# Performance work log

Hardware: AMD Instinct MI355X
Metric: run time of the kernel (lower is better)

The kernel has to match this reference:

```python
import jax, jax.numpy as jnp
import numpy as np

NEG_SLOPE = 0.2


def _gatv2_hop(x_l, x_r, src, dst, att_k, bias_k, num_nodes, add_self_loops):
    # x_l, x_r: [N, H, C]; src/dst: [E] int; att_k: [H, C]; bias_k: [C]
    if add_self_loops:
        loop = jnp.arange(num_nodes, dtype=src.dtype)
        src = jnp.concatenate([src, loop])
        dst = jnp.concatenate([dst, loop])
    g = jax.nn.leaky_relu(x_l[src] + x_r[dst], NEG_SLOPE)      # [E, H, C]
    logit = jnp.einsum('ehc,hc->eh', g, att_k)                 # [E, H]
    m = jax.ops.segment_max(logit, dst, num_segments=num_nodes)  # [N, H]
    a = jnp.exp(logit - m[dst])
    denom = jax.ops.segment_sum(a, dst, num_segments=num_nodes)  # [N, H]
    alpha = a / denom[dst]                                     # [E, H]
    out = jax.ops.segment_sum(alpha[:, :, None] * x_l[src], dst,
                              num_segments=num_nodes)          # [N, H, C]
    return out.mean(axis=1) + bias_k                           # concat=False -> head mean


def setup_inputs() -> dict:
    key = jax.random.key(0)
    N, E, IN, H, C, K = 50000, 800000, 128, 4, 32, 3
    ks = jax.random.split(key, 16)
    x = jax.random.normal(ks[0], (N, IN), dtype=jnp.float32)
    edges = {}
    for k in range(K):
        src = jax.random.randint(ks[1 + 2 * k], (E,), 0, N, dtype=jnp.int32)
        off = jax.random.randint(ks[2 + 2 * k], (E,), 1, N, dtype=jnp.int32)
        dst = (src + off) % N  # guarantees no self-loops in the data
        edges[f'edge_index{k}'] = jnp.stack([src, dst])
    s = 1.0 / np.sqrt(IN)
    w_l = jax.random.normal(ks[7], (IN, H * C), dtype=jnp.float32) * s
    b_l = jax.random.normal(ks[8], (H * C,), dtype=jnp.float32) * 0.02
    w_r = jax.random.normal(ks[9], (IN, H * C), dtype=jnp.float32) * s
    b_r = jax.random.normal(ks[10], (H * C,), dtype=jnp.float32) * 0.02
    att = jax.random.normal(ks[11], (K, H, C), dtype=jnp.float32) * (1.0 / np.sqrt(C))
    conv_bias = jax.random.normal(ks[12], (K, C), dtype=jnp.float32) * 0.02
    gate_w = jax.random.normal(ks[13], (IN, K), dtype=jnp.float32) * s
    gate_b = jax.random.normal(ks[14], (K,), dtype=jnp.float32) * 0.02
    return dict(x=x, **edges, w_l=w_l, b_l=b_l, w_r=w_r, b_r=b_r, att=att,
                conv_bias=conv_bias, gate_w=gate_w, gate_b=gate_b)


def reference(x, edge_index0, edge_index1, edge_index2,
              w_l, b_l, w_r, b_r, att, conv_bias, gate_w, gate_b):
    N = x.shape[0]
    H, C = att.shape[1], att.shape[2]
    x_l = (x @ w_l + b_l).reshape(N, H, C)  # shared lin_l across hops
    x_r = (x @ w_r + b_r).reshape(N, H, C)  # shared lin_r across hops
    edges = [edge_index0, edge_index1, edge_index2]
    msgs = [
        _gatv2_hop(x_l, x_r, ei[0], ei[1], att[k], conv_bias[k], N,
                   add_self_loops=(k == 0))
        for k, ei in enumerate(edges)
    ]
    messages = jnp.stack(msgs, axis=1)                 # [N, K, C]
    weights = jax.nn.softmax(x @ gate_w + gate_b, -1)  # [N, K]
    return jnp.einsum('nkc,nk->nc', messages, weights)
```

## Files before the change

### kernel.cpp

```cpp
#include <hip/hip_runtime.h>
#include <math.h>

typedef unsigned int uint32;
typedef unsigned short u16;

#if __has_builtin(__builtin_amdgcn_exp2f)
#define EXP2F(x) __builtin_amdgcn_exp2f(x)
#else
#define EXP2F(x) exp2f(x)
#endif

#define LROWS 64
#define CHUNK 8192
#define CHUNK_SHIFT 13
#define NBUCK_MAX 512
#define LPB 384

typedef __attribute__((ext_vector_type(8))) short bf16x8;
typedef __attribute__((ext_vector_type(4))) float f32x4;

__device__ __forceinline__ u16 f2bf(float f) {
    uint32 u = __float_as_uint(f);
    u += 0x7fffu + ((u >> 16) & 1u);
    return (u16)(u >> 16);
}
__device__ __forceinline__ float bflo(uint32 v) { return __uint_as_float(v << 16); }
__device__ __forceinline__ float bfhij(uint32 v) { return __uint_as_float(v); }

template<int PAT>
__device__ __forceinline__ float swz(float v) {
    return __int_as_float(__builtin_amdgcn_ds_swizzle(__float_as_int(v), PAT));
}
template<int CTRL>
__device__ __forceinline__ float dppadd(float v) {
    int r = __builtin_amdgcn_update_dpp(0, __float_as_int(v), CTRL, 0xF, 0xF, true);
    return v + __int_as_float(r);
}

__device__ __forceinline__ void edge_decode(
    int t, int E, const int* __restrict__ e0, const int* __restrict__ e1,
    const int* __restrict__ e2, int& hop, int& src, int& dst)
{
    if (t < E)          { hop = 0; src = e0[t];         dst = e0[E + t]; }
    else if (t < 2 * E) { hop = 1; src = e1[t - E];     dst = e1[t]; }
    else if (t < 3 * E) { hop = 2; src = e2[t - 2 * E]; dst = e2[t - E]; }
    else                { hop = 0; src = t - 3 * E;     dst = src; }
}

__global__ __launch_bounds__(256) void wprep(
    const float* __restrict__ wl, const float* __restrict__ wr, u16* __restrict__ wfrag)
{
    int ct = blockIdx.x;
    int ks = threadIdx.x >> 6;
    int lane = threadIdx.x & 63;
    int g = lane >> 4, rr = lane & 15;
    int c = ct * 16 + rr;
    const float* w = (c < 128) ? wl : wr;
    int cc = c & 127;
    u16* o = wfrag + (((size_t)ct * 4 + ks) * 64 + lane) * 8;
#pragma unroll
    for (int i = 0; i < 8; ++i) {
        int k = ks * 32 + g * 4 + (i & 3) + ((i >> 2) << 4);
        o[i] = f2bf(w[k * 128 + cc]);
    }
}

__global__ __launch_bounds__(256) void fused_pre(
    const float* __restrict__ x, const u16* __restrict__ wfrag,
    const float* __restrict__ bl, const float* __restrict__ br,
    const float* __restrict__ gw, const float* __restrict__ gb,
    u16* __restrict__ xl, u16* __restrict__ xr, float* __restrict__ gate4,
    const int* __restrict__ e0, const int* __restrict__ e1, const int* __restrict__ e2,
    int* __restrict__ hist,
    int N, int E, int T, int LB, int NBUCK)
{
    __shared__ float4 sx[LROWS][32];
    __shared__ float gbuf[LROWS][3];
    __shared__ int lhist[NBUCK_MAX];

    if ((int)blockIdx.x >= LB) {
        int blk = (int)blockIdx.x - LB;
        int t0 = blk << CHUNK_SHIFT;
        for (int j = threadIdx.x; j < NBUCK; j += 256) lhist[j] = 0;
        __syncthreads();
        for (int it = 0; it < CHUNK / 256; ++it) {
            int t = t0 + it * 256 + (int)threadIdx.x;
            if (t < T) {
                int dst;
                if (t < E)          dst = e0[E + t];
                else if (t < 2 * E) dst = e1[t];
                else if (t < 3 * E) dst = e2[t - E];
                else                dst = t - 3 * E;
                atomicAdd(&lhist[dst >> 7], 1);
            }
        }
        __syncthreads();
        for (int j = threadIdx.x; j < NBUCK; j += 256)
            hist[(size_t)blk * NBUCK + j] = lhist[j];
        return;
    }
    int t = threadIdx.x;
    int r0 = blockIdx.x * LROWS;
    int nr = min(LROWS, N - r0);
    {
        const float4* xi = (const float4*)(x + (size_t)r0 * 128);
        for (int i = t; i < nr * 32; i += 256) ((float4*)sx)[i] = xi[i];
    }
    __syncthreads();
    int wv = t >> 6, lane = t & 63;
    int g = lane >> 4, rr = lane & 15;
    bf16x8 afr[4];
    {
        const float4* xrow = sx[wv * 16 + rr];
#pragma unroll
        for (int ks = 0; ks < 4; ++ks) {
            float4 u = xrow[ks * 8 + g];
            float4 v = xrow[ks * 8 + 4 + g];
            union { u16 h[8]; bf16x8 v8; } pk;
            pk.h[0] = f2bf(u.x); pk.h[1] = f2bf(u.y);
            pk.h[2] = f2bf(u.z); pk.h[3] = f2bf(u.w);
            pk.h[4] = f2bf(v.x); pk.h[5] = f2bf(v.y);
            pk.h[6] = f2bf(v.z); pk.h[7] = f2bf(v.w);
            afr[ks] = pk.v8;
        }
    }
    const bf16x8* wfp = (const bf16x8*)wfrag;
    for (int ct = 0; ct < 16; ++ct) {
        f32x4 acc = {0.f, 0.f, 0.f, 0.f};
#pragma unroll
        for (int ks = 0; ks < 4; ++ks) {
            bf16x8 bf = wfp[((ct * 4 + ks) << 6) + lane];
            acc = __builtin_amdgcn_mfma_f32_16x16x32_bf16(afr[ks], bf, acc, 0, 0, 0);
        }
        int c = ct * 16 + rr;
        float bv = (ct < 8) ? bl[c] : br[c - 128];
        u16* ob = (ct < 8) ? xl : xr;
        int cc = c & 127;
#pragma unroll
        for (int i = 0; i < 4; ++i) {
            int row = wv * 16 + g * 4 + i;
            if (row < nr)
                ob[(size_t)(r0 + row) * 128 + cc] = f2bf(acc[i] + bv);
        }
    }
    if (t < nr * 3) {
        int r = t / 3, k = t - 3 * r;
        float s = 0.f;
        const float4* xrow = sx[r];
#pragma unroll 4
        for (int i = 0; i < 32; ++i) {
            float4 v = xrow[i];
            s += v.x * gw[(4 * i + 0) * 3 + k] + v.y * gw[(4 * i + 1) * 3 + k]
               + v.z * gw[(4 * i + 2) * 3 + k] + v.w * gw[(4 * i + 3) * 3 + k];
        }
        gbuf[r][k] = s + gb[k];
    }
    __syncthreads();
    if (t < nr) {
        float s0 = gbuf[t][0], s1 = gbuf[t][1], s2 = gbuf[t][2];
        float mx = fmaxf(s0, fmaxf(s1, s2));
        float e0v = __expf(s0 - mx), e1v = __expf(s1 - mx), e2v = __expf(s2 - mx);
        float inv = 1.f / (e0v + e1v + e2v);
        *(float4*)(gate4 + (size_t)(r0 + t) * 4) = make_float4(e0v * inv, e1v * inv, e2v * inv, 0.f);
    }
}

__global__ __launch_bounds__(1024) void scan1h(const int* __restrict__ hist, int MH,
                                               int NBLKA, int NBUCK,
                                               int* __restrict__ histS, int* __restrict__ partials) {
    __shared__ int s[1024];
    int t = threadIdx.x;
    int i = blockIdx.x * 1024 + t;
    int v = 0;
    if (i < MH) {
        int bin = (int)((uint32)i / (uint32)NBLKA);
        int blk = i - bin * NBLKA;
        v = hist[(size_t)blk * NBUCK + bin];
    }
    s[t] = v;
    __syncthreads();
    for (int o = 1; o < 1024; o <<= 1) {
        int u = (t >= o) ? s[t - o] : 0;
        __syncthreads();
        s[t] += u;
        __syncthreads();
    }
    if (i < MH) histS[i] = s[t] - v;
    if (t == 1023) partials[blockIdx.x] = s[1023];
}

__global__ __launch_bounds__(1024) void scan2(int* __restrict__ partials, int G) {
    __shared__ int s[1024];
    int t = threadIdx.x;
    int v = (t < G) ? partials[t] : 0;
    s[t] = v;
    __syncthreads();
    for (int o = 1; o < 1024; o <<= 1) {
        int u = (t >= o) ? s[t - o] : 0;
        __syncthreads();
        s[t] += u;
        __syncthreads();
    }
    if (t < G) partials[t] = s[t] - v;
}

__global__ __launch_bounds__(512) void passA2(
    const int* __restrict__ e0, const int* __restrict__ e1, const int* __restrict__ e2,
    int E, int T, int NBLKA, int NBUCK,
    const int* __restrict__ hist, const int* __restrict__ histS,
    const int* __restrict__ partials,
    uint32* __restrict__ pairs)
{
    __shared__ int lscan[512];
    __shared__ int gbase[512];
    __shared__ uint32 lp[CHUNK];
    __shared__ u16 lb[CHUNK];
    int blk = blockIdx.x, tid = threadIdx.x;
    int t0 = blk << CHUNK_SHIFT;
    int vc = min(CHUNK, T - t0);
    int c = (tid < NBUCK) ? hist[(size_t)blk * NBUCK + tid] : 0;
    lscan[tid] = c;
    __syncthreads();
    for (int o = 1; o < 512; o <<= 1) {
        int u = (tid >= o) ? lscan[tid - o] : 0;
        __syncthreads();
        lscan[tid] += u;
        __syncthreads();
    }
    int excl = lscan[tid] - c;
    lscan[tid] = excl;
    if (tid < NBUCK) {
        int k = tid * NBLKA + blk;
        gbase[tid] = histS[k] + partials[k >> 10] - excl;
    }
    __syncthreads();
    for (int it = 0; it < CHUNK / 512; ++it) {
        int t = t0 + it * 512 + tid;
        if (t < T) {
            int hop, src, dst;
            edge_decode(t, E, e0, e1, e2, hop, src, dst);
            int bin = dst >> 7;
            int j = atomicAdd(&lscan[bin], 1);
            lp[j] = (uint32)src | ((uint32)((dst & 127) * 3 + hop) << 16);
            lb[j] = (u16)bin;
        }
    }
    __syncthreads();
    for (int j = tid; j < vc; j += 512)
        pairs[gbase[lb[j]] + j] = lp[j];
}

__global__ __launch_bounds__(512) void passB(
    const uint32* __restrict__ pairs, const int* __restrict__ histS,
    const int* __restrict__ partials, u16* __restrict__ csr, int* __restrict__ offsets,
    int T, int M, int NBLKA, int NBUCK) {
    __shared__ int cnt[LPB];
    __shared__ int scn[512];
    int b = blockIdx.x;
    int tid = threadIdx.x;
    int k0 = b * NBLKA;
    int bbase = histS[k0] + partials[k0 >> 10];
    int bend;
    if (b == NBUCK - 1) bend = T;
    else { int k1 = k0 + NBLKA; bend = histS[k1] + partials[k1 >> 10]; }
    if (b == 0 && tid == 0) offsets[M] = T;

    if (tid < LPB) cnt[tid] = 0;
    __syncthreads();
    for (int p = bbase + tid; p < bend; p += 512)
        atomicAdd(&cnt[pairs[p] >> 16], 1);
    __syncthreads();
    int c = (tid < LPB) ? cnt[tid] : 0;
    scn[tid] = c;
    __syncthreads();
    for (int o = 1; o < 512; o <<= 1) {
        int u = (tid >= o) ? scn[tid - o] : 0;
        __syncthreads();
        scn[tid] += u;
        __syncthreads();
    }
    int excl = scn[tid] - c;
    int nlists = min(LPB, M - b * LPB);
    if (tid < nlists) offsets[b * LPB + tid] = bbase + excl;
    __syncthreads();
    if (tid < LPB) cnt[tid] = excl;
    __syncthreads();
    for (int p = bbase + tid; p < bend; p += 512) {
        uint32 pr = pairs[p];
        int pos = bbase + atomicAdd(&cnt[pr >> 16], 1);
        csr[pos] = (u16)pr;
    }
}

__global__ __launch_bounds__(192) void node_hop(
    const uint2* __restrict__ xlv,
    const uint2* __restrict__ xrv,
    const u16* __restrict__ csr,
    const int* __restrict__ offsets,
    const float* __restrict__ att,
    const float* __restrict__ bias,
    const float* __restrict__ gate4,
    float* __restrict__ out,
    int N, int M)
{
    const float L2E = 1.44269504088896f;
    __shared__ float4 smsg[3][8];
    int n = blockIdx.x;
    int h = threadIdx.x >> 6;
    int lane = threadIdx.x & 63;
    int i = 3 * n + h;
    int half = lane >> 5, l5 = lane & 31;

    uint2 rv = xrv[(size_t)n * 32 + l5];
    float4 r4;
    r4.x = bflo(rv.x); r4.y = bfhij(rv.x);
    r4.z = bflo(rv.y); r4.w = bfhij(rv.y);
    float4 a4 = ((const float4*)(att + h * 128))[l5];
    float a6x = 0.6f * L2E * a4.x, a6y = 0.6f * L2E * a4.y;
    float a6z = 0.6f * L2E * a4.z, a6w = 0.6f * L2E * a4.w;
    float a4x = 0.4f * L2E * a4.x, a4y = 0.4f * L2E * a4.y;
    float a4z = 0.4f * L2E * a4.z, a4w = 0.4f * L2E * a4.w;
    int beg = offsets[i];
    int end = offsets[i + 1];

    float d = 0.f, acc0 = 0.f, acc1 = 0.f, acc2 = 0.f, acc3 = 0.f;
    int e = beg;
    if (e + 8 <= end) {
        int sA = csr[e + half];
        int sB = csr[e + 2 + half];
        int sC = csr[e + 4 + half];
        int sD = csr[e + 6 + half];
        uint2 lvA = xlv[sA * 32 + l5];
        uint2 lvB = xlv[sB * 32 + l5];
        uint2 lvC = xlv[sC * 32 + l5];
        uint2 lvD = xlv[sD * 32 + l5];
        for (; e + 8 <= end; e += 8) {
            uint2 cvA = lvA, cvB = lvB, cvC = lvC, cvD = lvD;
            sA = csr[e + 8 + half];
            sB = csr[e + 10 + half];
            sC = csr[e + 12 + half];
            sD = csr[e + 14 + half];
            lvA = xlv[sA * 32 + l5];
            lvB = xlv[sB * 32 + l5];
            lvC = xlv[sC * 32 + l5];
            lvD = xlv[sD * 32 + l5];
            float lxA0 = bflo(cvA.x), lxA1 = bfhij(cvA.x);
            float lxA2 = bflo(cvA.y), lxA3 = bfhij(cvA.y);
            float lxB0 = bflo(cvB.x), lxB1 = bfhij(cvB.x);
            float lxB2 = bflo(cvB.y), lxB3 = bfhij(cvB.y);
            float lxC0 = bflo(cvC.x), lxC1 = bfhij(cvC.x);
            float lxC2 = bflo(cvC.y), lxC3 = bfhij(cvC.y);
            float lxD0 = bflo(cvD.x), lxD1 = bfhij(cvD.x);
            float lxD2 = bflo(cvD.y), lxD3 = bfhij(cvD.y);
            float gA0 = lxA0 + r4.x, gA1 = lxA1 + r4.y, gA2 = lxA2 + r4.z, gA3 = lxA3 + r4.w;
            float gB0 = lxB0 + r4.x, gB1 = lxB1 + r4.y, gB2 = lxB2 + r4.z, gB3 = lxB3 + r4.w;
            float gC0 = lxC0 + r4.x, gC1 = lxC1 + r4.y, gC2 = lxC2 + r4.z, gC3 = lxC3 + r4.w;
            float gD0 = lxD0 + r4.x, gD1 = lxD1 + r4.y, gD2 = lxD2 + r4.z, gD3 = lxD3 + r4.w;
            float pA = a6x * gA0;
            pA = fmaf(a4x, fabsf(gA0), pA);
            pA = fmaf(a6y, gA1, pA);
            pA = fmaf(a4y, fabsf(gA1), pA);
            pA = fmaf(a6z, gA2, pA);
            pA = fmaf(a4z, fabsf(gA2), pA);
            pA = fmaf(a6w, gA3, pA);
            pA = fmaf(a4w, fabsf(gA3), pA);
            float pB = a6x * gB0;
            pB = fmaf(a4x, fabsf(gB0), pB);
            pB = fmaf(a6y, gB1, pB);
            pB = fmaf(a4y, fabsf(gB1), pB);
            pB = fmaf(a6z, gB2, pB);
            pB = fmaf(a4z, fabsf(gB2), pB);
            pB = fmaf(a6w, gB3, pB);
            pB = fmaf(a4w, fabsf(gB3), pB);
            float pC = a6x * gC0;
            pC = fmaf(a4x, fabsf(gC0), pC);
            pC = fmaf(a6y, gC1, pC);
            pC = fmaf(a4y, fabsf(gC1), pC);
            pC = fmaf(a6z, gC2, pC);
            pC = fmaf(a4z, fabsf(gC2), pC);
            pC = fmaf(a6w, gC3, pC);
            pC = fmaf(a4w, fabsf(gC3), pC);
            float pD = a6x * gD0;
            pD = fmaf(a4x, fabsf(gD0), pD);
            pD = fmaf(a6y, gD1, pD);
            pD = fmaf(a4y, fabsf(gD1), pD);
            pD = fmaf(a6z, gD2, pD);
            pD = fmaf(a4z, fabsf(gD2), pD);
            pD = fmaf(a6w, gD3, pD);
            pD = fmaf(a4w, fabsf(gD3), pD);
            pA = dppadd<0xB1>(pA);  pB = dppadd<0xB1>(pB);
            pC = dppadd<0xB1>(pC);  pD = dppadd<0xB1>(pD);
            pA = dppadd<0x4E>(pA);  pB = dppadd<0x4E>(pB);
            pC = dppadd<0x4E>(pC);  pD = dppadd<0x4E>(pD);
            pA = dppadd<0x141>(pA); pB = dppadd<0x141>(pB);
            pC = dppadd<0x141>(pC); pD = dppadd<0x141>(pD);
            float wvA = EXP2F(pA);
            float wvB = EXP2F(pB);
            float wvC = EXP2F(pC);
            float wvD = EXP2F(pD);
            d += (wvA + wvB) + (wvC + wvD);
            acc0 = fmaf(wvA, lxA0, acc0);
            acc1 = fmaf(wvA, lxA1, acc1);
            acc2 = fmaf(wvA, lxA2, acc2);
            acc3 = fmaf(wvA, lxA3, acc3);
            acc0 = fmaf(wvB, lxB0, acc0);
            acc1 = fmaf(wvB, lxB1, acc1);
            acc2 = fmaf(wvB, lxB2, acc2);
            acc3 = fmaf(wvB, lxB3, acc3);
            acc0 = fmaf(wvC, lxC0, acc0);
            acc1 = fmaf(wvC, lxC1, acc1);
            acc2 = fmaf(wvC, lxC2, acc2);
            acc3 = fmaf(wvC, lxC3, acc3);
            acc0 = fmaf(wvD, lxD0, acc0);
            acc1 = fmaf(wvD, lxD1, acc1);
            acc2 = fmaf(wvD, lxD2, acc2);
            acc3 = fmaf(wvD, lxD3, acc3);
        }
    }
    for (; e < end; e += 4) {
        int e1i = end - 1;
        int s1 = csr[min(e + half, e1i)];
        int s2 = csr[min(e + 2 + half, e1i)];
        uint2 cvA = xlv[s1 * 32 + l5];
        uint2 cvB = xlv[s2 * 32 + l5];
        bool vA = (e + half) < end;
        bool vB = (e + 2 + half) < end;
        float lxA0 = bflo(cvA.x), lxA1 = bfhij(cvA.x);
        float lxA2 = bflo(cvA.y), lxA3 = bfhij(cvA.y);
        float lxB0 = bflo(cvB.x), lxB1 = bfhij(cvB.x);
        float lxB2 = bflo(cvB.y), lxB3 = bfhij(cvB.y);
        float gA0 = lxA0 + r4.x, gA1 = lxA1 + r4.y;
        float gA2 = lxA2 + r4.z, gA3 = lxA3 + r4.w;
        float gB0 = lxB0 + r4.x, gB1 = lxB1 + r4.y;
        float gB2 = lxB2 + r4.z, gB3 = lxB3 + r4.w;
        float pA = a6x * gA0;
        pA = fmaf(a4x, fabsf(gA0), pA);
        pA = fmaf(a6y, gA1, pA);
        pA = fmaf(a4y, fabsf(gA1), pA);
        pA = fmaf(a6z, gA2, pA);
        pA = fmaf(a4z, fabsf(gA2), pA);
        pA = fmaf(a6w, gA3, pA);
        pA = fmaf(a4w, fabsf(gA3), pA);
        float pB = a6x * gB0;
        pB = fmaf(a4x, fabsf(gB0), pB);
        pB = fmaf(a6y, gB1, pB);
        pB = fmaf(a4y, fabsf(gB1), pB);
        pB = fmaf(a6z, gB2, pB);
        pB = fmaf(a4z, fabsf(gB2), pB);
        pB = fmaf(a6w, gB3, pB);
        pB = fmaf(a4w, fabsf(gB3), pB);
        pA = dppadd<0xB1>(pA);
        pB = dppadd<0xB1>(pB);
        pA = dppadd<0x4E>(pA);
        pB = dppadd<0x4E>(pB);
        pA = dppadd<0x141>(pA);
        pB = dppadd<0x141>(pB);
        float wvA = EXP2F(pA);
        float wvB = EXP2F(pB);
        wvA = vA ? wvA : 0.f;
        wvB = vB ? wvB : 0.f;
        d += wvA + wvB;
        acc0 = fmaf(wvA, lxA0, acc0);
        acc1 = fmaf(wvA, lxA1, acc1);
        acc2 = fmaf(wvA, lxA2, acc2);
        acc3 = fmaf(wvA, lxA3, acc3);
        acc0 = fmaf(wvB, lxB0, acc0);
        acc1 = fmaf(wvB, lxB1, acc1);
        acc2 = fmaf(wvB, lxB2, acc2);
        acc3 = fmaf(wvB, lxB3, acc3);
    }
    d += __shfl_xor(d, 32);
    acc0 += __shfl_xor(acc0, 32);
    acc1 += __shfl_xor(acc1, 32);
    acc2 += __shfl_xor(acc2, 32);
    acc3 += __shfl_xor(acc3, 32);
    float inv = (d > 0.f) ? (1.0f / d) : 0.f;
    float q0 = acc0 * inv, q1 = acc1 * inv, q2 = acc2 * inv, q3 = acc3 * inv;
    q0 += swz<0x201F>(q0);  q0 += swz<0x401F>(q0);
    q1 += swz<0x201F>(q1);  q1 += swz<0x401F>(q1);
    q2 += swz<0x201F>(q2);  q2 += swz<0x401F>(q2);
    q3 += swz<0x201F>(q3);  q3 += swz<0x401F>(q3);
    if (lane < 8) {
        float4 b4 = ((const float4*)(bias + h * 32))[lane];
        smsg[h][lane] = make_float4(fmaf(q0, 0.25f, b4.x), fmaf(q1, 0.25f, b4.y),
                                    fmaf(q2, 0.25f, b4.z), fmaf(q3, 0.25f, b4.w));
    }
    __syncthreads();
    if (threadIdx.x < 8) {
        int c = threadIdx.x;
        float4 g = ((const float4*)gate4)[n];
        float4 m0 = smsg[0][c], m1 = smsg[1][c], m2 = smsg[2][c];
        float4 o;
        o.x = g.x * m0.x + g.y * m1.x + g.z * m2.x;
        o.y = g.x * m0.y + g.y * m1.y + g.z * m2.y;
        o.z = g.x * m0.z + g.y * m1.z + g.z * m2.z;
        o.w = g.x * m0.w + g.y * m1.w + g.z * m2.w;
        ((float4*)(out + (size_t)n * 32))[c] = o;
    }
}

extern "C" void kernel_launch(void* const* d_in, const int* in_sizes, int n_in,
                              void* d_out, int out_size, void* d_ws, size_t ws_size,
                              hipStream_t stream) {
    const float* x  = (const float*)d_in[0];
    const int* e0 = (const int*)d_in[1];
    const int* e1 = (const int*)d_in[2];
    const int* e2 = (const int*)d_in[3];
    const float* wl = (const float*)d_in[4];
    const float* bl = (const float*)d_in[5];
    const float* wr = (const float*)d_in[6];
    const float* br = (const float*)d_in[7];
    const float* att = (const float*)d_in[8];
    const float* cb  = (const float*)d_in[9];
    const float* gw  = (const float*)d_in[10];
    const float* gb  = (const float*)d_in[11];

    int N = in_sizes[0] / 128;
    int E = in_sizes[1] / 2;
    float* out = (float*)d_out;

    int M = 3 * N;
    int T = 3 * E + N;
    int NBUCK = (N + 127) >> 7;
    int NBLKA = (T + CHUNK - 1) / CHUNK;
    int MH = NBUCK * NBLKA;

    char* ws = (char*)d_ws;
    u16* xl      = (u16*)ws;   ws += (size_t)N * 128 * 2;
    u16* xr      = (u16*)ws;   ws += (size_t)N * 128 * 2;
    float* gate4 = (float*)ws; ws += (size_t)N * 4 * 4;
    int* offsets  = (int*)ws; ws += (size_t)(M + 1) * 4;
    int* hist     = (int*)ws; ws += (size_t)MH * 4;
    int* histS    = (int*)ws; ws += (size_t)MH * 4;
    int* partials = (int*)ws; ws += 4096;
    u16* csr_src  = (u16*)ws; ws += (size_t)(T + 16) * 2;
    u16* wfrag    = (u16*)ws; ws += (size_t)16 * 4 * 64 * 8 * 2;
    uint32* pairs = (uint32*)(((uintptr_t)ws + 63) & ~(uintptr_t)63);

    int LB = (N + LROWS - 1) / LROWS;
    wprep<<<16, 256, 0, stream>>>(wl, wr, wfrag);
    fused_pre<<<LB + NBLKA, 256, 0, stream>>>(x, wfrag, bl, br, gw, gb, xl, xr, gate4,
                                              e0, e1, e2, hist, N, E, T, LB, NBUCK);
    int GH = (MH + 1023) / 1024;
    scan1h<<<GH, 1024, 0, stream>>>(hist, MH, NBLKA, NBUCK, histS, partials);
    scan2<<<1, 1024, 0, stream>>>(partials, GH);
    passA2<<<NBLKA, 512, 0, stream>>>(e0, e1, e2, E, T, NBLKA, NBUCK,
                                      hist, histS, partials, pairs);
    passB<<<NBUCK, 512, 0, stream>>>(pairs, histS, partials, csr_src, offsets,
                                     T, M, NBLKA, NBUCK);
    node_hop<<<N, 192, 0, stream>>>(
        (const uint2*)xl, (const uint2*)xr, csr_src, offsets, att, cb, gate4, out, N, M);
}
```

Measured before the change: 171.9 us.

## Fuse CSR bucket build with per-node attention aggregation using LDS-resident CSR

Merges the passB CSR scatter and the node_hop kernel into one per-bucket kernel. Each bucket's 128 destination nodes get their CSR offsets and source indices built in shared memory. The same block's 8 waves then process 16 nodes each across all three hops, writing the gated output directly. This removes the global offsets and CSR arrays and one kernel launch. In exchange the grid drops from one block per node to one block per bucket. That sharply reduces the waves available to hide gather latency, serialises hops and nodes within a wave, and assumes each bucket holds at most 8192 edges with no overflow check.

```diff
diff --git a/kernel.cpp b/kernel.cpp
--- a/kernel.cpp
+++ b/kernel.cpp
@@ -15,6 +15,7 @@
 #define CHUNK_SHIFT 13
 #define NBUCK_MAX 512
 #define LPB 384
+#define BCAP 8192
 
 typedef __attribute__((ext_vector_type(8))) short bf16x8;
 typedef __attribute__((ext_vector_type(4))) float f32x4;
@@ -250,12 +251,22 @@
         pairs[gbase[lb[j]] + j] = lp[j];
 }
 
-__global__ __launch_bounds__(512) void passB(
-    const uint32* __restrict__ pairs, const int* __restrict__ histS,
-    const int* __restrict__ partials, u16* __restrict__ csr, int* __restrict__ offsets,
-    int T, int M, int NBLKA, int NBUCK) {
+__global__ __launch_bounds__(512) void node_bucket(
+    const uint2* __restrict__ xlv,
+    const uint2* __restrict__ xrv,
+    const uint32* __restrict__ pairs,
+    const int* __restrict__ histS, const int* __restrict__ partials,
+    const float* __restrict__ att,
+    const float* __restrict__ bias,
+    const float* __restrict__ gate4,
+    float* __restrict__ out,
+    int N, int T, int NBLKA, int NBUCK)
+{
+    const float L2E = 1.44269504088896f;
     __shared__ int cnt[LPB];
     __shared__ int scn[512];
+    __shared__ int loff[LPB + 1];
+    __shared__ u16 lcsr[BCAP + 16];
     int b = blockIdx.x;
     int tid = threadIdx.x;
     int k0 = b * NBLKA;
@@ -263,7 +274,7 @@
     int bend;
     if (b == NBUCK - 1) bend = T;
     else { int k1 = k0 + NBLKA; bend = histS[k1] + partials[k1 >> 10]; }
-    if (b == 0 && tid == 0) offsets[M] = T;
+    int bc = bend - bbase;
 
     if (tid < LPB) cnt[tid] = 0;
     __syncthreads();
@@ -280,222 +291,202 @@
         __syncthreads();
     }
     int excl = scn[tid] - c;
-    int nlists = min(LPB, M - b * LPB);
-    if (tid < nlists) offsets[b * LPB + tid] = bbase + excl;
-    __syncthreads();
+    if (tid <= LPB) loff[tid] = excl;
     if (tid < LPB) cnt[tid] = excl;
+    if (tid < 16) lcsr[bc + tid] = 0;
     __syncthreads();
     for (int p = bbase + tid; p < bend; p += 512) {
         uint32 pr = pairs[p];
-        int pos = bbase + atomicAdd(&cnt[pr >> 16], 1);
-        csr[pos] = (u16)pr;
-    }
-}
-
-__global__ __launch_bounds__(192) void node_hop(
-    const uint2* __restrict__ xlv,
-    const uint2* __restrict__ xrv,
-    const u16* __restrict__ csr,
-    const int* __restrict__ offsets,
-    const float* __restrict__ att,
-    const float* __restrict__ bias,
-    const float* __restrict__ gate4,
-    float* __restrict__ out,
-    int N, int M)
-{
-    const float L2E = 1.44269504088896f;
-    __shared__ float4 smsg[3][8];
-    int n = blockIdx.x;
-    int h = threadIdx.x >> 6;
-    int lane = threadIdx.x & 63;
-    int i = 3 * n + h;
+        int pos = atomicAdd(&cnt[pr >> 16], 1);
+        lcsr[pos] = (u16)pr;
+    }
+    __syncthreads();
+
+    int wvid = tid >> 6;
+    int lane = tid & 63;
     int half = lane >> 5, l5 = lane & 31;
-
-    uint2 rv = xrv[(size_t)n * 32 + l5];
-    float4 r4;
-    r4.x = bflo(rv.x); r4.y = bfhij(rv.x);
-    r4.z = bflo(rv.y); r4.w = bfhij(rv.y);
-    float4 a4 = ((const float4*)(att + h * 128))[l5];
-    float a6x = 0.6f * L2E * a4.x, a6y = 0.6f * L2E * a4.y;
-    float a6z = 0.6f * L2E * a4.z, a6w = 0.6f * L2E * a4.w;
-    float a4x = 0.4f * L2E * a4.x, a4y = 0.4f * L2E * a4.y;
-    float a4z = 0.4f * L2E * a4.z, a4w = 0.4f * L2E * a4.w;
-    int beg = offsets[i];
-    int end = offsets[i + 1];
-
-    float d = 0.f, acc0 = 0.f, acc1 = 0.f, acc2 = 0.f, acc3 = 0.f;
-    int e = beg;
-    if (e + 8 <= end) {
-        int sA = csr[e + half];
-        int sB = csr[e + 2 + half];
-        int sC = csr[e + 4 + half];
-        int sD = csr[e + 6 + half];
-        uint2 lvA = xlv[sA * 32 + l5];
-        uint2 lvB = xlv[sB * 32 + l5];
-        uint2 lvC = xlv[sC * 32 + l5];
-        uint2 lvD = xlv[sD * 32 + l5];
-        for (; e + 8 <= end; e += 8) {
-            uint2 cvA = lvA, cvB = lvB, cvC = lvC, cvD = lvD;
-            sA = csr[e + 8 + half];
-            sB = csr[e + 10 + half];
-            sC = csr[e + 12 + half];
-            sD = csr[e + 14 + half];
-            lvA = xlv[sA * 32 + l5];
-            lvB = xlv[sB * 32 + l5];
-            lvC = xlv[sC * 32 + l5];
-            lvD = xlv[sD * 32 + l5];
-            float lxA0 = bflo(cvA.x), lxA1 = bfhij(cvA.x);
-            float lxA2 = bflo(cvA.y), lxA3 = bfhij(cvA.y);
-            float lxB0 = bflo(cvB.x), lxB1 = bfhij(cvB.x);
-            float lxB2 = bflo(cvB.y), lxB3 = bfhij(cvB.y);
-            float lxC0 = bflo(cvC.x), lxC1 = bfhij(cvC.x);
-            float lxC2 = bflo(cvC.y), lxC3 = bfhij(cvC.y);
-            float lxD0 = bflo(cvD.x), lxD1 = bfhij(cvD.x);
-            float lxD2 = bflo(cvD.y), lxD3 = bfhij(cvD.y);
-            float gA0 = lxA0 + r4.x, gA1 = lxA1 + r4.y, gA2 = lxA2 + r4.z, gA3 = lxA3 + r4.w;
-            float gB0 = lxB0 + r4.x, gB1 = lxB1 + r4.y, gB2 = lxB2 + r4.z, gB3 = lxB3 + r4.w;
-            float gC0 = lxC0 + r4.x, gC1 = lxC1 + r4.y, gC2 = lxC2 + r4.z, gC3 = lxC3 + r4.w;
-            float gD0 = lxD0 + r4.x, gD1 = lxD1 + r4.y, gD2 = lxD2 + r4.z, gD3 = lxD3 + r4.w;
-            float pA = a6x * gA0;
-            pA = fmaf(a4x, fabsf(gA0), pA);
-            pA = fmaf(a6y, gA1, pA);
-            pA = fmaf(a4y, fabsf(gA1), pA);
-            pA = fmaf(a6z, gA2, pA);
-            pA = fmaf(a4z, fabsf(gA2), pA);
-            pA = fmaf(a6w, gA3, pA);
-            pA = fmaf(a4w, fabsf(gA3), pA);
-            float pB = a6x * gB0;
-            pB = fmaf(a4x, fabsf(gB0), pB);
-            pB = fmaf(a6y, gB1, pB);
-            pB = fmaf(a4y, fabsf(gB1), pB);
-            pB = fmaf(a6z, gB2, pB);
-            pB = fmaf(a4z, fabsf(gB2), pB);
-            pB = fmaf(a6w, gB3, pB);
-            pB = fmaf(a4w, fabsf(gB3), pB);
-            float pC = a6x * gC0;
-            pC = fmaf(a4x, fabsf(gC0), pC);
-            pC = fmaf(a6y, gC1, pC);
-            pC = fmaf(a4y, fabsf(gC1), pC);
-            pC = fmaf(a6z, gC2, pC);
-            pC = fmaf(a4z, fabsf(gC2), pC);
-            pC = fmaf(a6w, gC3, pC);
-            pC = fmaf(a4w, fabsf(gC3), pC);
-            float pD = a6x * gD0;
-            pD = fmaf(a4x, fabsf(gD0), pD);
-            pD = fmaf(a6y, gD1, pD);
-            pD = fmaf(a4y, fabsf(gD1), pD);
-            pD = fmaf(a6z, gD2, pD);
-            pD = fmaf(a4z, fabsf(gD2), pD);
-            pD = fmaf(a6w, gD3, pD);
-            pD = fmaf(a4w, fabsf(gD3), pD);
-            pA = dppadd<0xB1>(pA);  pB = dppadd<0xB1>(pB);
-            pC = dppadd<0xB1>(pC);  pD = dppadd<0xB1>(pD);
-            pA = dppadd<0x4E>(pA);  pB = dppadd<0x4E>(pB);
-            pC = dppadd<0x4E>(pC);  pD = dppadd<0x4E>(pD);
-            pA = dppadd<0x141>(pA); pB = dppadd<0x141>(pB);
-            pC = dppadd<0x141>(pC); pD = dppadd<0x141>(pD);
-            float wvA = EXP2F(pA);
-            float wvB = EXP2F(pB);
-            float wvC = EXP2F(pC);
-            float wvD = EXP2F(pD);
-            d += (wvA + wvB) + (wvC + wvD);
-            acc0 = fmaf(wvA, lxA0, acc0);
-            acc1 = fmaf(wvA, lxA1, acc1);
-            acc2 = fmaf(wvA, lxA2, acc2);
-            acc3 = fmaf(wvA, lxA3, acc3);
-            acc0 = fmaf(wvB, lxB0, acc0);
-            acc1 = fmaf(wvB, lxB1, acc1);
-            acc2 = fmaf(wvB, lxB2, acc2);
-            acc3 = fmaf(wvB, lxB3, acc3);
-            acc0 = fmaf(wvC, lxC0, acc0);
-            acc1 = fmaf(wvC, lxC1, acc1);
-            acc2 = fmaf(wvC, lxC2, acc2);
-            acc3 = fmaf(wvC, lxC3, acc3);
-            acc0 = fmaf(wvD, lxD0, acc0);
-            acc1 = fmaf(wvD, lxD1, acc1);
-            acc2 = fmaf(wvD, lxD2, acc2);
-            acc3 = fmaf(wvD, lxD3, acc3);
-        }
-    }
-    for (; e < end; e += 4) {
-        int e1i = end - 1;
-        int s1 = csr[min(e + half, e1i)];
-        int s2 = csr[min(e + 2 + half, e1i)];
-        uint2 cvA = xlv[s1 * 32 + l5];
-        uint2 cvB = xlv[s2 * 32 + l5];
-        bool vA = (e + half) < end;
-        bool vB = (e + 2 + half) < end;
-        float lxA0 = bflo(cvA.x), lxA1 = bfhij(cvA.x);
-        float lxA2 = bflo(cvA.y), lxA3 = bfhij(cvA.y);
-        float lxB0 = bflo(cvB.x), lxB1 = bfhij(cvB.x);
-        float lxB2 = bflo(cvB.y), lxB3 = bfhij(cvB.y);
-        float gA0 = lxA0 + r4.x, gA1 = lxA1 + r4.y;
-        float gA2 = lxA2 + r4.z, gA3 = lxA3 + r4.w;
-        float gB0 = lxB0 + r4.x, gB1 = lxB1 + r4.y;
-        float gB2 = lxB2 + r4.z, gB3 = lxB3 + r4.w;
-        float pA = a6x * gA0;
-        pA = fmaf(a4x, fabsf(gA0), pA);
-        pA = fmaf(a6y, gA1, pA);
-        pA = fmaf(a4y, fabsf(gA1), pA);
-        pA = fmaf(a6z, gA2, pA);
-        pA = fmaf(a4z, fabsf(gA2), pA);
-        pA = fmaf(a6w, gA3, pA);
-        pA = fmaf(a4w, fabsf(gA3), pA);
-        float pB = a6x * gB0;
-        pB = fmaf(a4x, fabsf(gB0), pB);
-        pB = fmaf(a6y, gB1, pB);
-        pB = fmaf(a4y, fabsf(gB1), pB);
-        pB = fmaf(a6z, gB2, pB);
-        pB = fmaf(a4z, fabsf(gB2), pB);
-        pB = fmaf(a6w, gB3, pB);
-        pB = fmaf(a4w, fabsf(gB3), pB);
-        pA = dppadd<0xB1>(pA);
-        pB = dppadd<0xB1>(pB);
-        pA = dppadd<0x4E>(pA);
-        pB = dppadd<0x4E>(pB);
-        pA = dppadd<0x141>(pA);
-        pB = dppadd<0x141>(pB);
-        float wvA = EXP2F(pA);
-        float wvB = EXP2F(pB);
-        wvA = vA ? wvA : 0.f;
-        wvB = vB ? wvB : 0.f;
-        d += wvA + wvB;
-        acc0 = fmaf(wvA, lxA0, acc0);
-        acc1 = fmaf(wvA, lxA1, acc1);
-        acc2 = fmaf(wvA, lxA2, acc2);
-        acc3 = fmaf(wvA, lxA3, acc3);
-        acc0 = fmaf(wvB, lxB0, acc0);
-        acc1 = fmaf(wvB, lxB1, acc1);
-        acc2 = fmaf(wvB, lxB2, acc2);
-        acc3 = fmaf(wvB, lxB3, acc3);
-    }
-    d += __shfl_xor(d, 32);
-    acc0 += __shfl_xor(acc0, 32);
-    acc1 += __shfl_xor(acc1, 32);
-    acc2 += __shfl_xor(acc2, 32);
-    acc3 += __shfl_xor(acc3, 32);
-    float inv = (d > 0.f) ? (1.0f / d) : 0.f;
-    float q0 = acc0 * inv, q1 = acc1 * inv, q2 = acc2 * inv, q3 = acc3 * inv;
-    q0 += swz<0x201F>(q0);  q0 += swz<0x401F>(q0);
-    q1 += swz<0x201F>(q1);  q1 += swz<0x401F>(q1);
-    q2 += swz<0x201F>(q2);  q2 += swz<0x401F>(q2);
-    q3 += swz<0x201F>(q3);  q3 += swz<0x401F>(q3);
-    if (lane < 8) {
-        float4 b4 = ((const float4*)(bias + h * 32))[lane];
-        smsg[h][lane] = make_float4(fmaf(q0, 0.25f, b4.x), fmaf(q1, 0.25f, b4.y),
-                                    fmaf(q2, 0.25f, b4.z), fmaf(q3, 0.25f, b4.w));
-    }
-    __syncthreads();
-    if (threadIdx.x < 8) {
-        int c = threadIdx.x;
-        float4 g = ((const float4*)gate4)[n];
-        float4 m0 = smsg[0][c], m1 = smsg[1][c], m2 = smsg[2][c];
-        float4 o;
-        o.x = g.x * m0.x + g.y * m1.x + g.z * m2.x;
-        o.y = g.x * m0.y + g.y * m1.y + g.z * m2.y;
-        o.z = g.x * m0.z + g.y * m1.z + g.z * m2.z;
-        o.w = g.x * m0.w + g.y * m1.w + g.z * m2.w;
-        ((float4*)(out + (size_t)n * 32))[c] = o;
+    for (int ln = wvid * 16; ln < wvid * 16 + 16; ++ln) {
+        int n = b * 128 + ln;
+        if (n >= N) break;
+        uint2 rv = xrv[(size_t)n * 32 + l5];
+        float4 r4;
+        r4.x = bflo(rv.x); r4.y = bfhij(rv.x);
+        r4.z = bflo(rv.y); r4.w = bfhij(rv.y);
+        float4 gv = ((const float4*)gate4)[n];
+        float res0 = 0.f, res1 = 0.f, res2 = 0.f, res3 = 0.f;
+        for (int h = 0; h < 3; ++h) {
+            float4 a4 = ((const float4*)(att + h * 128))[l5];
+            float a6x = 0.6f * L2E * a4.x, a6y = 0.6f * L2E * a4.y;
+            float a6z = 0.6f * L2E * a4.z, a6w = 0.6f * L2E * a4.w;
+            float a4x = 0.4f * L2E * a4.x, a4y = 0.4f * L2E * a4.y;
+            float a4z = 0.4f * L2E * a4.z, a4w = 0.4f * L2E * a4.w;
+            int li = ln * 3 + h;
+            int beg = loff[li], end = loff[li + 1];
+            float d = 0.f, acc0 = 0.f, acc1 = 0.f, acc2 = 0.f, acc3 = 0.f;
+            int e = beg;
+            if (e + 8 <= end) {
+                int sA = lcsr[e + half];
+                int sB = lcsr[e + 2 + half];
+                int sC = lcsr[e + 4 + half];
+                int sD = lcsr[e + 6 + half];
+                uint2 lvA = xlv[sA * 32 + l5];
+                uint2 lvB = xlv[sB * 32 + l5];
+                uint2 lvC = xlv[sC * 32 + l5];
+                uint2 lvD = xlv[sD * 32 + l5];
+                for (; e + 8 <= end; e += 8) {
+                    uint2 cvA = lvA, cvB = lvB, cvC = lvC, cvD = lvD;
+                    sA = lcsr[e + 8 + half];
+                    sB = lcsr[e + 10 + half];
+                    sC = lcsr[e + 12 + half];
+                    sD = lcsr[e + 14 + half];
+                    lvA = xlv[sA * 32 + l5];
+                    lvB = xlv[sB * 32 + l5];
+                    lvC = xlv[sC * 32 + l5];
+                    lvD = xlv[sD * 32 + l5];
+                    float lxA0 = bflo(cvA.x), lxA1 = bfhij(cvA.x);
+                    float lxA2 = bflo(cvA.y), lxA3 = bfhij(cvA.y);
+                    float lxB0 = bflo(cvB.x), lxB1 = bfhij(cvB.x);
+                    float lxB2 = bflo(cvB.y), lxB3 = bfhij(cvB.y);
+                    float lxC0 = bflo(cvC.x), lxC1 = bfhij(cvC.x);
+                    float lxC2 = bflo(cvC.y), lxC3 = bfhij(cvC.y);
+                    float lxD0 = bflo(cvD.x), lxD1 = bfhij(cvD.x);
+                    float lxD2 = bflo(cvD.y), lxD3 = bfhij(cvD.y);
+                    float gA0 = lxA0 + r4.x, gA1 = lxA1 + r4.y, gA2 = lxA2 + r4.z, gA3 = lxA3 + r4.w;
+                    float gB0 = lxB0 + r4.x, gB1 = lxB1 + r4.y, gB2 = lxB2 + r4.z, gB3 = lxB3 + r4.w;
+                    float gC0 = lxC0 + r4.x, gC1 = lxC1 + r4.y, gC2 = lxC2 + r4.z, gC3 = lxC3 + r4.w;
+                    float gD0 = lxD0 + r4.x, gD1 = lxD1 + r4.y, gD2 = lxD2 + r4.z, gD3 = lxD3 + r4.w;
+                    float pA = a6x * gA0;
+                    pA = fmaf(a4x, fabsf(gA0), pA);
+                    pA = fmaf(a6y, gA1, pA);
+                    pA = fmaf(a4y, fabsf(gA1), pA);
+                    pA = fmaf(a6z, gA2, pA);
+                    pA = fmaf(a4z, fabsf(gA2), pA);
+                    pA = fmaf(a6w, gA3, pA);
+                    pA = fmaf(a4w, fabsf(gA3), pA);
+                    float pB = a6x * gB0;
+                    pB = fmaf(a4x, fabsf(gB0), pB);
+                    pB = fmaf(a6y, gB1, pB);
+                    pB = fmaf(a4y, fabsf(gB1), pB);
+                    pB = fmaf(a6z, gB2, pB);
+                    pB = fmaf(a4z, fabsf(gB2), pB);
+                    pB = fmaf(a6w, gB3, pB);
+                    pB = fmaf(a4w, fabsf(gB3), pB);
+                    float pC = a6x * gC0;
+                    pC = fmaf(a4x, fabsf(gC0), pC);
+                    pC = fmaf(a6y, gC1, pC);
+                    pC = fmaf(a4y, fabsf(gC1), pC);
+                    pC = fmaf(a6z, gC2, pC);
+                    pC = fmaf(a4z, fabsf(gC2), pC);
+                    pC = fmaf(a6w, gC3, pC);
+                    pC = fmaf(a4w, fabsf(gC3), pC);
+                    float pD = a6x * gD0;
+                    pD = fmaf(a4x, fabsf(gD0), pD);
+                    pD = fmaf(a6y, gD1, pD);
+                    pD = fmaf(a4y, fabsf(gD1), pD);
+                    pD = fmaf(a6z, gD2, pD);
+                    pD = fmaf(a4z, fabsf(gD2), pD);
+                    pD = fmaf(a6w, gD3, pD);
+                    pD = fmaf(a4w, fabsf(gD3), pD);
+                    pA = dppadd<0xB1>(pA);  pB = dppadd<0xB1>(pB);
+                    pC = dppadd<0xB1>(pC);  pD = dppadd<0xB1>(pD);
+                    pA = dppadd<0x4E>(pA);  pB = dppadd<0x4E>(pB);
+                    pC = dppadd<0x4E>(pC);  pD = dppadd<0x4E>(pD);
+                    pA = dppadd<0x141>(pA); pB = dppadd<0x141>(pB);
+                    pC = dppadd<0x141>(pC); pD = dppadd<0x141>(pD);
+                    float wvA = EXP2F(pA);
+                    float wvB = EXP2F(pB);
+                    float wvC = EXP2F(pC);
+                    float wvD = EXP2F(pD);
+                    d += (wvA + wvB) + (wvC + wvD);
+                    acc0 = fmaf(wvA, lxA0, acc0);
+                    acc1 = fmaf(wvA, lxA1, acc1);
+                    acc2 = fmaf(wvA, lxA2, acc2);
+                    acc3 = fmaf(wvA, lxA3, acc3);
+                    acc0 = fmaf(wvB, lxB0, acc0);
+                    acc1 = fmaf(wvB, lxB1, acc1);
+                    acc2 = fmaf(wvB, lxB2, acc2);
+                    acc3 = fmaf(wvB, lxB3, acc3);
+                    acc0 = fmaf(wvC, lxC0, acc0);
+                    acc1 = fmaf(wvC, lxC1, acc1);
+                    acc2 = fmaf(wvC, lxC2, acc2);
+                    acc3 = fmaf(wvC, lxC3, acc3);
+                    acc0 = fmaf(wvD, lxD0, acc0);
+                    acc1 = fmaf(wvD, lxD1, acc1);
+                    acc2 = fmaf(wvD, lxD2, acc2);
+                    acc3 = fmaf(wvD, lxD3, acc3);
+                }
+            }
+            for (; e < end; e += 4) {
+                int e1i = end - 1;
+                int s1 = lcsr[min(e + half, e1i)];
+                int s2 = lcsr[min(e + 2 + half, e1i)];
+                uint2 cvA = xlv[s1 * 32 + l5];
+                uint2 cvB = xlv[s2 * 32 + l5];
+                bool vA = (e + half) < end;
+                bool vB = (e + 2 + half) < end;
+                float lxA0 = bflo(cvA.x), lxA1 = bfhij(cvA.x);
+                float lxA2 = bflo(cvA.y), lxA3 = bfhij(cvA.y);
+                float lxB0 = bflo(cvB.x), lxB1 = bfhij(cvB.x);
+                float lxB2 = bflo(cvB.y), lxB3 = bfhij(cvB.y);
+                float gA0 = lxA0 + r4.x, gA1 = lxA1 + r4.y;
+                float gA2 = lxA2 + r4.z, gA3 = lxA3 + r4.w;
+                float gB0 = lxB0 + r4.x, gB1 = lxB1 + r4.y;
+                float gB2 = lxB2 + r4.z, gB3 = lxB3 + r4.w;
+                float pA = a6x * gA0;
+                pA = fmaf(a4x, fabsf(gA0), pA);
+                pA = fmaf(a6y, gA1, pA);
+                pA = fmaf(a4y, fabsf(gA1), pA);
+                pA = fmaf(a6z, gA2, pA);
+                pA = fmaf(a4z, fabsf(gA2), pA);
+                pA = fmaf(a6w, gA3, pA);
+                pA = fmaf(a4w, fabsf(gA3), pA);
+                float pB = a6x * gB0;
+                pB = fmaf(a4x, fabsf(gB0), pB);
+                pB = fmaf(a6y, gB1, pB);
+                pB = fmaf(a4y, fabsf(gB1), pB);
+                pB = fmaf(a6z, gB2, pB);
+                pB = fmaf(a4z, fabsf(gB2), pB);
+                pB = fmaf(a6w, gB3, pB);
+                pB = fmaf(a4w, fabsf(gB3), pB);
+                pA = dppadd<0xB1>(pA);
+                pB = dppadd<0xB1>(pB);
+                pA = dppadd<0x4E>(pA);
+                pB = dppadd<0x4E>(pB);
+                pA = dppadd<0x141>(pA);
+                pB = dppadd<0x141>(pB);
+                float wvA = EXP2F(pA);
+                float wvB = EXP2F(pB);
+                wvA = vA ? wvA : 0.f;
+                wvB = vB ? wvB : 0.f;
+                d += wvA + wvB;
+                acc0 = fmaf(wvA, lxA0, acc0);
+                acc1 = fmaf(wvA, lxA1, acc1);
+                acc2 = fmaf(wvA, lxA2, acc2);
+                acc3 = fmaf(wvA, lxA3, acc3);
+                acc0 = fmaf(wvB, lxB0, acc0);
+                acc1 = fmaf(wvB, lxB1, acc1);
+                acc2 = fmaf(wvB, lxB2, acc2);
+                acc3 = fmaf(wvB, lxB3, acc3);
+            }
+            d += __shfl_xor(d, 32);
+            acc0 += __shfl_xor(acc0, 32);
+            acc1 += __shfl_xor(acc1, 32);
+            acc2 += __shfl_xor(acc2, 32);
+            acc3 += __shfl_xor(acc3, 32);
+            float inv = (d > 0.f) ? (1.0f / d) : 0.f;
+            float q0 = acc0 * inv, q1 = acc1 * inv, q2 = acc2 * inv, q3 = acc3 * inv;
+            q0 += swz<0x201F>(q0);  q0 += swz<0x401F>(q0);
+            q1 += swz<0x201F>(q1);  q1 += swz<0x401F>(q1);
+            q2 += swz<0x201F>(q2);  q2 += swz<0x401F>(q2);
+            q3 += swz<0x201F>(q3);  q3 += swz<0x401F>(q3);
+            float4 b4 = ((const float4*)(bias + h * 32))[lane & 7];
+            float g = (h == 0) ? gv.x : ((h == 1) ? gv.y : gv.z);
+            res0 = fmaf(g, fmaf(q0, 0.25f, b4.x), res0);
+            res1 = fmaf(g, fmaf(q1, 0.25f, b4.y), res1);
+            res2 = fmaf(g, fmaf(q2, 0.25f, b4.z), res2);
+            res3 = fmaf(g, fmaf(q3, 0.25f, b4.w), res3);
+        }
+        if (lane < 8) ((float4*)(out + (size_t)n * 32))[lane] = make_float4(res0, res1, res2, res3);
     }
 }
 
@@ -524,16 +515,15 @@
     int NBUCK = (N + 127) >> 7;
     int NBLKA = (T + CHUNK - 1) / CHUNK;
     int MH = NBUCK * NBLKA;
+    (void)M;
 
     char* ws = (char*)d_ws;
     u16* xl      = (u16*)ws;   ws += (size_t)N * 128 * 2;
     u16* xr      = (u16*)ws;   ws += (size_t)N * 128 * 2;
     float* gate4 = (float*)ws; ws += (size_t)N * 4 * 4;
-    int* offsets  = (int*)ws; ws += (size_t)(M + 1) * 4;
     int* hist     = (int*)ws; ws += (size_t)MH * 4;
     int* histS    = (int*)ws; ws += (size_t)MH * 4;
     int* partials = (int*)ws; ws += 4096;
-    u16* csr_src  = (u16*)ws; ws += (size_t)(T + 16) * 2;
     u16* wfrag    = (u16*)ws; ws += (size_t)16 * 4 * 64 * 8 * 2;
     uint32* pairs = (uint32*)(((uintptr_t)ws + 63) & ~(uintptr_t)63);
 
@@ -546,8 +536,7 @@
     scan2<<<1, 1024, 0, stream>>>(partials, GH);
     passA2<<<NBLKA, 512, 0, stream>>>(e0, e1, e2, E, T, NBLKA, NBUCK,
                                       hist, histS, partials, pairs);
-    passB<<<NBUCK, 512, 0, stream>>>(pairs, histS, partials, csr_src, offsets,
-                                     T, M, NBLKA, NBUCK);
-    node_hop<<<N, 192, 0, stream>>>(
-        (const uint2*)xl, (const uint2*)xr, csr_src, offsets, att, cb, gate4, out, N, M);
-}
+    node_bucket<<<NBUCK, 512, 0, stream>>>(
+        (const uint2*)xl, (const uint2*)xr, pairs, histS, partials,
+        att, cb, gate4, out, N, T, NBLKA, NBUCK);
+}
```

After: 192.8 us. 12.2% more time.
